# Performance work log

Measured on AMD Instinct MI355X. Metric: run time of the kernel, lower is better.

The kernel has to match this reference:

```python
import jax, jax.numpy as jnp
import numpy as np

B, S, D, H, DH = 2, 2048, 1024, 16, 64
LN_EPS = 1e-5

def _layernorm(x, g, b):
    mu = jnp.mean(x, axis=-1, keepdims=True)
    var = jnp.mean(jnp.square(x - mu), axis=-1, keepdims=True)
    return (x - mu) * jax.lax.rsqrt(var + LN_EPS) * g + b

def setup_inputs() -> dict:
    key = jax.random.key(0)
    ks = jax.random.split(key, 12)
    s = 0.02
    return {
        'x': jax.random.normal(ks[0], (B, S, D), jnp.float32),
        'attention_mask': jnp.zeros((B, S), jnp.bool_),
        'Wq': jax.random.normal(ks[1], (H, D, DH), jnp.float32) * s,
        'bq': jnp.zeros((H, DH), jnp.float32),
        'Wk': jax.random.normal(ks[2], (H, D, DH), jnp.float32) * s,
        'bk': jnp.zeros((H, DH), jnp.float32),
        'Wv': jax.random.normal(ks[3], (H, D, DH), jnp.float32) * s,
        'bv': jnp.zeros((H, DH), jnp.float32),
        'ln_g': jnp.ones((D,), jnp.float32),
        'ln_b': jnp.zeros((D,), jnp.float32),
        'W1': jax.random.normal(ks[4], (D, 4 * D), jnp.float32) * s,
        'b1': jnp.zeros((4 * D,), jnp.float32),
        'W2': jax.random.normal(ks[5], (4 * D, D), jnp.float32) * s,
        'b2': jnp.zeros((D,), jnp.float32),
    }

def reference(x, attention_mask, Wq, bq, Wk, bk, Wv, bv, ln_g, ln_b, W1, b1, W2, b2):
    # NOTE: source has a typo bug ('attentoin_score'), so the attention_mask is
    # computed-then-discarded; softmax is applied to the UNMASKED scaled scores.
    dh = Wq.shape[-1]
    q = jnp.einsum('bsd,hde->bhse', x, Wq) + bq[:, None, :]  # [B,H,S,dh]
    k = jnp.einsum('bsd,hde->bhse', x, Wk) + bk[:, None, :]
    v = jnp.einsum('bsd,hde->bhse', x, Wv) + bv[:, None, :]
    scores = jnp.einsum('bhse,bhte->bhst', q, k) / jnp.sqrt(jnp.float32(dh))
    attn = jax.nn.softmax(scores, axis=-1)
    o = jnp.einsum('bhst,bhte->bhse', attn, v)  # [B,H,S,dh]
    b_, h_, s_, e_ = o.shape
    # concat heads along last dim == transpose then reshape
    mha = jnp.transpose(o, (0, 2, 1, 3)).reshape(b_, s_, h_ * e_)
    h1 = _layernorm(x + mha, ln_g, ln_b)
    ffn = jax.nn.relu(h1 @ W1 + b1) @ W2 + b2
    return _layernorm(h1 + ffn, ln_g, ln_b)
```

## Files before the change

kernel.cpp:

```cpp
#include <hip/hip_runtime.h>

#define DEVI __device__ __forceinline__

typedef __attribute__((ext_vector_type(8))) __bf16 bf16x8;
typedef __attribute__((ext_vector_type(4))) float f32x4;
typedef __attribute__((ext_vector_type(4))) unsigned short u16x4;
typedef __attribute__((ext_vector_type(8))) unsigned short u16x8;

static DEVI unsigned short f2bf(float f) {
  unsigned int i = __float_as_uint(f);
  i += 0x7fffu + ((i >> 16) & 1u);
  return (unsigned short)(i >> 16);
}

static DEVI unsigned short f2bfh(float f) {
  union { __bf16 h; unsigned short u; } c;
  c.h = (__bf16)f;
  return c.u;
}

static DEVI float bf2f(unsigned short u) {
  return __uint_as_float((unsigned int)u << 16);
}

static DEVI f32x4 mfma16x16x32(bf16x8 a, bf16x8 b, f32x4 c) {
  return __builtin_amdgcn_mfma_f32_16x16x32_bf16(a, b, c, 0, 0, 0);
}

static DEVI void async_ld16(const void* g, void* lds) {
  __builtin_amdgcn_global_load_lds(
      (const __attribute__((address_space(1))) void*)g,
      (__attribute__((address_space(3))) void*)lds, 16, 0, 0);
}

template <int BN, int OUT_MODE, bool RELU>
static DEVI void gemm_bt_core(const unsigned short* __restrict__ A, int lda,
                              const unsigned short* __restrict__ Bt, int ldb,
                              int K, int m0, int n0,
                              const float* __restrict__ bias,
                              void* __restrict__ Cp, int ldc,
                              const float* __restrict__ bq,
                              const float* __restrict__ bk,
                              const float* __restrict__ bv,
                              unsigned short* __restrict__ qo,
                              unsigned short* __restrict__ ko,
                              unsigned short* __restrict__ vo) {
  constexpr int MT = (BN == 128) ? 4 : 2;
  constexpr int NT = 4;
  __shared__ __align__(16) unsigned short As[128 * 32];
  __shared__ __align__(16) unsigned short Bs[BN * 32];

  const int tid = threadIdx.x;
  const int w = tid >> 6, l = tid & 63;
  const int lr = l & 15, lq = l >> 4;
  const int wm0 = (BN == 128) ? ((w >> 1) * 64) : (w * 32);
  const int wn0 = (BN == 128) ? ((w & 1) * 64) : 0;
  const int lrow = l >> 2;
  const int lcol = (l & 3) * 8;

  f32x4 acc[MT][NT];
#pragma unroll
  for (int i = 0; i < MT; ++i)
#pragma unroll
    for (int j = 0; j < NT; ++j) acc[i][j] = (f32x4){0.f, 0.f, 0.f, 0.f};

  for (int kb = 0; kb < K; kb += 32) {
#pragma unroll
    for (int p = 0; p < 2; ++p) {
      const int r0 = p * 64 + w * 16;
      async_ld16(A + (size_t)(m0 + r0 + lrow) * lda + kb + lcol, As + r0 * 32);
    }
#pragma unroll
    for (int p = 0; p < BN / 64; ++p) {
      const int r0 = p * 64 + w * 16;
      async_ld16(Bt + (size_t)(n0 + r0 + lrow) * ldb + kb + lcol, Bs + r0 * 32);
    }
    __syncthreads();

    bf16x8 af[MT], bfr[NT];
#pragma unroll
    for (int mt = 0; mt < MT; ++mt)
      af[mt] = *(const bf16x8*)(As + (wm0 + mt * 16 + lr) * 32 + lq * 8);
#pragma unroll
    for (int nt = 0; nt < NT; ++nt)
      bfr[nt] = *(const bf16x8*)(Bs + (wn0 + nt * 16 + lr) * 32 + lq * 8);
#pragma unroll
    for (int mt = 0; mt < MT; ++mt)
#pragma unroll
      for (int nt = 0; nt < NT; ++nt)
        acc[mt][nt] = mfma16x16x32(af[mt], bfr[nt], acc[mt][nt]);
    __syncthreads();
  }

#pragma unroll
  for (int mt = 0; mt < MT; ++mt) {
    const int grow = m0 + wm0 + mt * 16 + lq * 4;
#pragma unroll
    for (int nt = 0; nt < NT; ++nt) {
      const int gcol = n0 + wn0 + nt * 16 + lr;
      if (OUT_MODE == 2) {
        const int which = gcol >> 10;
        const int h = (gcol >> 6) & 15;
        const int e = gcol & 63;
        const float* bp = (which == 0) ? bq : (which == 1) ? bk : bv;
        const float bvv = bp[gcol & 1023];
#pragma unroll
        for (int r = 0; r < 4; ++r) {
          const int row = grow + r;
          const int b_ = row >> 11, s_ = row & 2047;
          const size_t base = (size_t)((b_ << 4) + h) * 131072;
          const float val = acc[mt][nt][r] + bvv;
          if (which == 0) {
            qo[base + (size_t)s_ * 64 + e] = f2bf(val);
          } else if (which == 1) {
            const int o = e >> 3;
            const int pos = (((o ^ (s_ & 7)) << 3) | (e & 7));
            ko[base + (size_t)s_ * 64 + pos] = f2bf(val * 0.18033688011112f);
          } else {
            const int t = s_ >> 6, k64 = s_ & 63;
            const int kap = (k64 & 15) * 4 + (k64 >> 4);
            const int pos = (((kap >> 3) ^ (e & 7)) << 3) | (kap & 7);
            vo[base + (size_t)e * 2048 + t * 64 + pos] = f2bf(val);
          }
        }
      } else if (OUT_MODE == 3) {
#pragma unroll
        for (int r = 0; r < 4; ++r)
          ((unsigned short*)Cp)[(size_t)(grow + r) * ldc + gcol] =
              f2bf(acc[mt][nt][r]);
      } else {
        const float bvv = bias[gcol];
#pragma unroll
        for (int r = 0; r < 4; ++r) {
          float val = acc[mt][nt][r] + bvv;
          if (RELU) val = fmaxf(val, 0.f);
          if (OUT_MODE == 1)
            ((unsigned short*)Cp)[(size_t)(grow + r) * ldc + gcol] = f2bf(val);
          else
            ((float*)Cp)[(size_t)(grow + r) * ldc + gcol] = val;
        }
      }
    }
  }
}

__global__ __launch_bounds__(256) void k_gemm_qkv(
    const unsigned short* __restrict__ xb, const unsigned short* __restrict__ Wt,
    const float* __restrict__ bq, const float* __restrict__ bk,
    const float* __restrict__ bv, unsigned short* __restrict__ qo,
    unsigned short* __restrict__ ko, unsigned short* __restrict__ vo) {
  gemm_bt_core<128, 2, false>(xb, 1024, Wt, 1024, 1024, blockIdx.x * 128,
                              blockIdx.y * 128, nullptr, nullptr, 0, bq, bk, bv,
                              qo, ko, vo);
}

__global__ __launch_bounds__(256) void k_ffn1(
    const unsigned short* __restrict__ h1b, const unsigned short* __restrict__ W1t,
    const float* __restrict__ b1, unsigned short* __restrict__ f1) {
  gemm_bt_core<128, 1, true>(h1b, 1024, W1t, 1024, 1024, blockIdx.x * 128,
                             blockIdx.y * 128, b1, f1, 4096, nullptr, nullptr,
                             nullptr, nullptr, nullptr, nullptr);
}

__global__ __launch_bounds__(256) void k_ffn2(
    const unsigned short* __restrict__ f1, const unsigned short* __restrict__ W2t,
    unsigned short* __restrict__ pbase) {
  const int z = blockIdx.z;
  unsigned short* p = pbase + (size_t)z * 4194304;
  gemm_bt_core<128, 3, false>(f1 + z * 1024, 4096, W2t + z * 1024, 4096, 1024,
                              blockIdx.x * 128, blockIdx.y * 128, nullptr, p,
                              1024, nullptr, nullptr, nullptr, nullptr, nullptr,
                              nullptr);
}

static DEVI void tr64(const float* __restrict__ s, int sld,
                      unsigned short* __restrict__ d, int dld) {
  __shared__ float t[64][65];
  const int tr = threadIdx.x >> 4;
  const int tc4 = (threadIdx.x & 15) * 4;
#pragma unroll
  for (int i = 0; i < 4; ++i) {
    f32x4 v = *(const f32x4*)(s + (size_t)(i * 16 + tr) * sld + tc4);
#pragma unroll
    for (int j = 0; j < 4; ++j) t[i * 16 + tr][tc4 + j] = v[j];
  }
  __syncthreads();
#pragma unroll
  for (int i = 0; i < 4; ++i) {
    const int c = i * 16 + tr;
    u16x4 pk;
#pragma unroll
    for (int j = 0; j < 4; ++j) pk[j] = f2bf(t[tc4 + j][c]);
    *(u16x4*)(d + (size_t)c * dld + tc4) = pk;
  }
}

__global__ __launch_bounds__(256) void k_prep(
    const float* __restrict__ x, const float* __restrict__ Wq,
    const float* __restrict__ Wk, const float* __restrict__ Wv,
    const float* __restrict__ W1, const float* __restrict__ W2,
    unsigned short* __restrict__ xb, unsigned short* __restrict__ wqkvt,
    unsigned short* __restrict__ w1t, unsigned short* __restrict__ w2t) {
  const int bid = blockIdx.x;
  if (bid < 1024) {
    const size_t i0 = ((size_t)bid * 256 + threadIdx.x) * 16;
#pragma unroll
    for (int c = 0; c < 4; ++c) {
      f32x4 v = *(const f32x4*)(x + i0 + c * 4);
      u16x4 pk;
#pragma unroll
      for (int j = 0; j < 4; ++j) pk[j] = f2bf(v[j]);
      *(u16x4*)(xb + i0 + c * 4) = pk;
    }
  } else if (bid < 1792) {
    const int t = bid - 1024;
    const int bx = t & 15, by = t >> 4;
    const int which = by >> 4, h = by & 15;
    const float* W = (which == 0) ? Wq : (which == 1) ? Wk : Wv;
    const float* s = W + (size_t)h * 65536;
    unsigned short* d = wqkvt + (size_t)(which * 1024 + h * 64) * 1024;
    const int r0 = bx * 64;
    tr64(s + (size_t)r0 * 64, 64, d + r0, 1024);
  } else if (bid < 2816) {
    const int t = bid - 1792;
    const int bx = t & 15, by = t >> 4;
    const int r0 = bx * 64, c0 = by * 64;
    tr64(W1 + (size_t)r0 * 4096 + c0, 4096, w1t + (size_t)c0 * 1024 + r0, 1024);
  } else {
    const int t = bid - 2816;
    const int bx = t & 63, by = t >> 6;
    const int r0 = bx * 64, c0 = by * 64;
    tr64(W2 + (size_t)r0 * 1024 + c0, 1024, w2t + (size_t)c0 * 4096 + r0, 4096);
  }
}

__global__ __launch_bounds__(512) void k_attn(
    const unsigned short* __restrict__ q, const unsigned short* __restrict__ ks,
    const unsigned short* __restrict__ vp, unsigned short* __restrict__ mha) {
  const int bid = blockIdx.x;
  const int bh = (bid & 7) * 4 + ((bid >> 3) >> 4);
  const int qt = (bid >> 3) & 15;
  const int b = bh >> 4, h = bh & 15;
  const int tid = threadIdx.x;
  const int w = tid >> 6, l = tid & 63;
  const int lr = l & 15, lq = l >> 4, l7 = lr & 7;

  __shared__ __align__(16) unsigned short Ks[2][64 * 64];
  __shared__ __align__(16) unsigned short Vt[2][64 * 64];
  __shared__ __align__(16) unsigned short Ps[8][16][72];

  const size_t bho = (size_t)bh * 131072;
  const int q0 = qt * 128 + w * 16;

  bf16x8 qf0, qf1;
  {
    const unsigned short* qp = q + bho + (size_t)(q0 + lr) * 64 + lq * 8;
    qf0 = *(const bf16x8*)qp;
    qf1 = *(const bf16x8*)(qp + 32);
  }

  f32x4 l_acc[4];
  f32x4 o[4];
#pragma unroll
  for (int i = 0; i < 4; ++i) {
    l_acc[i] = (f32x4){0.f, 0.f, 0.f, 0.f};
    o[i] = (f32x4){0.f, 0.f, 0.f, 0.f};
  }

  const unsigned short* kg = ks + bho;
  const unsigned short* vg = vp + bho;
  const int srow = l >> 3, scol = (l & 7) * 8;
  const int r0 = w * 8;

  async_ld16(kg + (size_t)(r0 + srow) * 64 + scol, &Ks[0][r0 * 64]);
  async_ld16(vg + (size_t)(r0 + srow) * 2048 + scol, &Vt[0][r0 * 64]);
  __syncthreads();

  for (int kt = 0; kt < 32; ++kt) {
    const int cur = kt & 1, nxt = cur ^ 1;
    if (kt + 1 < 32) {
      const int k1 = (kt + 1) * 64;
      async_ld16(kg + (size_t)(k1 + r0 + srow) * 64 + scol, &Ks[nxt][r0 * 64]);
      async_ld16(vg + (size_t)(r0 + srow) * 2048 + k1 + scol, &Vt[nxt][r0 * 64]);
    }

    bf16x8 kf[4][2];
#pragma unroll
    for (int ct = 0; ct < 4; ++ct)
#pragma unroll
      for (int hh = 0; hh < 2; ++hh)
        kf[ct][hh] = *(const bf16x8*)&Ks[cur][(ct * 16 + lr) * 64 +
                                             (((hh << 2) | lq) ^ l7) * 8];
    f32x4 s[4];
#pragma unroll
    for (int ct = 0; ct < 4; ++ct) {
      f32x4 t = {0.f, 0.f, 0.f, 0.f};
      t = mfma16x16x32(qf0, kf[ct][0], t);
      t = mfma16x16x32(qf1, kf[ct][1], t);
      s[ct] = t;
    }

#pragma unroll
    for (int r = 0; r < 4; ++r) {
      f32x4 pe;
#pragma unroll
      for (int ct = 0; ct < 4; ++ct)
        pe[ct] = __builtin_amdgcn_exp2f(s[ct][r]);
      l_acc[r] += pe;
      u16x4 pk;
#pragma unroll
      for (int ct = 0; ct < 4; ++ct) pk[ct] = f2bfh(pe[ct]);
      *(u16x4*)&Ps[w][lq * 4 + r][lr * 4] = pk;
    }
    __asm__ volatile("" ::: "memory");

    bf16x8 vf[4][2];
#pragma unroll
    for (int dt = 0; dt < 4; ++dt)
#pragma unroll
      for (int hh = 0; hh < 2; ++hh)
        vf[dt][hh] = *(const bf16x8*)&Vt[cur][(dt * 16 + lr) * 64 +
                                             (((hh << 2) | lq) ^ l7) * 8];
    bf16x8 pf0 = *(const bf16x8*)&Ps[w][lr][lq * 8];
    bf16x8 pf1 = *(const bf16x8*)&Ps[w][lr][32 + lq * 8];
#pragma unroll
    for (int dt = 0; dt < 4; ++dt) {
      o[dt] = mfma16x16x32(pf0, vf[dt][0], o[dt]);
      o[dt] = mfma16x16x32(pf1, vf[dt][1], o[dt]);
    }
    __syncthreads();
  }

#pragma unroll
  for (int r = 0; r < 4; ++r) {
    f32x4 la = l_acc[r];
    float sd = la[0] + la[1] + la[2] + la[3];
    sd += __shfl_xor(sd, 1);
    sd += __shfl_xor(sd, 2);
    sd += __shfl_xor(sd, 4);
    sd += __shfl_xor(sd, 8);
    const float inv = 1.f / sd;
    unsigned short* op =
        mha + ((size_t)b * 2048 + q0 + lq * 4 + r) * 1024 + h * 64 + lr;
    op[0] = f2bfh(o[0][r] * inv);
    op[16] = f2bfh(o[1][r] * inv);
    op[32] = f2bfh(o[2][r] * inv);
    op[48] = f2bfh(o[3][r] * inv);
  }
}

__global__ __launch_bounds__(256) void k_add_ln(const float* __restrict__ a,
                                                const unsigned short* __restrict__ b,
                                                const float* __restrict__ g,
                                                const float* __restrict__ be,
                                                unsigned short* __restrict__ outb) {
  const int row = blockIdx.x;
  const int tid = threadIdx.x;
  const size_t base = (size_t)row * 1024 + tid * 4;
  f32x4 va = *(const f32x4*)(a + base);
  u16x4 ub = *(const u16x4*)(b + base);
  f32x4 xx;
  float s = 0.f, q = 0.f;
#pragma unroll
  for (int i = 0; i < 4; ++i) {
    xx[i] = va[i] + bf2f(ub[i]);
    s += xx[i];
    q += xx[i] * xx[i];
  }
#pragma unroll
  for (int off = 1; off < 64; off <<= 1) {
    s += __shfl_xor(s, off);
    q += __shfl_xor(q, off);
  }
  __shared__ float ss[4], qs[4];
  const int w = tid >> 6;
  if ((tid & 63) == 0) { ss[w] = s; qs[w] = q; }
  __syncthreads();
  s = ss[0] + ss[1] + ss[2] + ss[3];
  q = qs[0] + qs[1] + qs[2] + qs[3];
  const float mean = s * (1.f / 1024.f);
  const float var = q * (1.f / 1024.f) - mean * mean;
  const float rstd = rsqrtf(var + 1e-5f);
  f32x4 vg = *(const f32x4*)(g + tid * 4);
  f32x4 vbe = *(const f32x4*)(be + tid * 4);
  u16x4 pk;
#pragma unroll
  for (int i = 0; i < 4; ++i)
    pk[i] = f2bf((xx[i] - mean) * rstd * vg[i] + vbe[i]);
  *(u16x4*)(outb + base) = pk;
}

__global__ __launch_bounds__(256) void k_add_ln4(
    const unsigned short* __restrict__ h1b, const unsigned short* __restrict__ pb,
    const float* __restrict__ cb, const float* __restrict__ g,
    const float* __restrict__ be, float* __restrict__ out) {
  const int row = blockIdx.x;
  const int tid = threadIdx.x;
  const size_t base = (size_t)row * 1024 + tid * 4;
  u16x4 uh = *(const u16x4*)(h1b + base);
  u16x4 up[4];
#pragma unroll
  for (int z = 0; z < 4; ++z)
    up[z] = *(const u16x4*)(pb + base + (size_t)z * 4194304);
  f32x4 vcb = *(const f32x4*)(cb + tid * 4);
  f32x4 xx;
  float s = 0.f, q = 0.f;
#pragma unroll
  for (int i = 0; i < 4; ++i) {
    float v = bf2f(uh[i]) + vcb[i];
#pragma unroll
    for (int z = 0; z < 4; ++z) v += bf2f(up[z][i]);
    xx[i] = v;
    s += v;
    q += v * v;
  }
#pragma unroll
  for (int off = 1; off < 64; off <<= 1) {
    s += __shfl_xor(s, off);
    q += __shfl_xor(q, off);
  }
  __shared__ float ss[4], qs[4];
  const int w = tid >> 6;
  if ((tid & 63) == 0) { ss[w] = s; qs[w] = q; }
  __syncthreads();
  s = ss[0] + ss[1] + ss[2] + ss[3];
  q = qs[0] + qs[1] + qs[2] + qs[3];
  const float mean = s * (1.f / 1024.f);
  const float var = q * (1.f / 1024.f) - mean * mean;
  const float rstd = rsqrtf(var + 1e-5f);
  f32x4 vg = *(const f32x4*)(g + tid * 4);
  f32x4 vbe = *(const f32x4*)(be + tid * 4);
  f32x4 ov;
#pragma unroll
  for (int i = 0; i < 4; ++i) ov[i] = (xx[i] - mean) * rstd * vg[i] + vbe[i];
  *(f32x4*)(out + base) = ov;
}

extern "C" void kernel_launch(void* const* d_in, const int* in_sizes, int n_in,
                              void* d_out, int out_size, void* d_ws,
                              size_t ws_size, hipStream_t stream) {
  const float* x = (const float*)d_in[0];
  const float* Wq = (const float*)d_in[2];
  const float* bq = (const float*)d_in[3];
  const float* Wk = (const float*)d_in[4];
  const float* bk = (const float*)d_in[5];
  const float* Wv = (const float*)d_in[6];
  const float* bv = (const float*)d_in[7];
  const float* lg = (const float*)d_in[8];
  const float* lb = (const float*)d_in[9];
  const float* W1 = (const float*)d_in[10];
  const float* b1 = (const float*)d_in[11];
  const float* W2 = (const float*)d_in[12];
  const float* b2 = (const float*)d_in[13];

  char* ws = (char*)d_ws;
  const size_t MB = 1024 * 1024;
  unsigned short* qb = (unsigned short*)(ws + 0);
  unsigned short* kb = (unsigned short*)(ws + 8 * MB);
  unsigned short* vp = (unsigned short*)(ws + 16 * MB);
  unsigned short* f1 = (unsigned short*)(ws + 0);
  unsigned short* xb = (unsigned short*)(ws + 32 * MB);
  unsigned short* pb = (unsigned short*)(ws + 32 * MB);
  unsigned short* mha = (unsigned short*)(ws + 40 * MB);
  unsigned short* h1b = (unsigned short*)(ws + 64 * MB);
  unsigned short* wqkvt = (unsigned short*)(ws + 72 * MB);
  unsigned short* w1t = (unsigned short*)(ws + 78 * MB);
  unsigned short* w2t = (unsigned short*)(ws + 86 * MB);

  k_prep<<<dim3(3840), 256, 0, stream>>>(x, Wq, Wk, Wv, W1, W2, xb, wqkvt, w1t,
                                         w2t);
  k_gemm_qkv<<<dim3(32, 24), 256, 0, stream>>>(xb, wqkvt, bq, bk, bv, qb, kb, vp);
  k_attn<<<dim3(512), 512, 0, stream>>>(qb, kb, vp, mha);
  k_add_ln<<<dim3(4096), 256, 0, stream>>>(x, mha, lg, lb, h1b);
  k_ffn1<<<dim3(32, 32), 256, 0, stream>>>(h1b, w1t, b1, f1);
  k_ffn2<<<dim3(32, 8, 4), 256, 0, stream>>>(f1, w2t, pb);
  k_add_ln4<<<dim3(4096), 256, 0, stream>>>(h1b, pb, b2, lg, lb, (float*)d_out);
}
```

Before: 325.3 us.

## Replace GEMM core with 256x256 double-buffered pipelined tile and XCD-aware block mapping

Replaces the 128x128 single-buffered GEMM core with a 256x256 tile over 8 waves and a 64-wide K step. LDS is double-buffered and XOR-swizzled, async loads are interleaved with quadrant MFMA phases, and explicit vmcnt waits, barriers and setprio are used. Blocks are remapped so tiles sharing A/B rows land on the same XCD, aiming at higher arithmetic intensity, overlapped loads and better L2 reuse. The grid shrinks to 192/256/256 blocks, so wave quantization and occupancy with 128 KB LDS per block are risks.

```diff
diff --git a/kernel.cpp b/kernel.cpp
--- a/kernel.cpp
+++ b/kernel.cpp
@@ -33,11 +33,16 @@
       (__attribute__((address_space(3))) void*)lds, 16, 0, 0);
 }
 
-template <int BN, int OUT_MODE, bool RELU>
-static DEVI void gemm_bt_core(const unsigned short* __restrict__ A, int lda,
+static DEVI void wg_barrier() {
+  __asm__ volatile("" ::: "memory");
+  __builtin_amdgcn_s_barrier();
+  __asm__ volatile("" ::: "memory");
+}
+
+template <int OUT_MODE, bool RELU>
+static DEVI void gemm256_core(const unsigned short* __restrict__ A, int lda,
                               const unsigned short* __restrict__ Bt, int ldb,
-                              int K, int m0, int n0,
-                              const float* __restrict__ bias,
+                              int m0, int n0, const float* __restrict__ bias,
                               void* __restrict__ Cp, int ldc,
                               const float* __restrict__ bq,
                               const float* __restrict__ bk,
@@ -45,132 +50,213 @@
                               unsigned short* __restrict__ qo,
                               unsigned short* __restrict__ ko,
                               unsigned short* __restrict__ vo) {
-  constexpr int MT = (BN == 128) ? 4 : 2;
-  constexpr int NT = 4;
-  __shared__ __align__(16) unsigned short As[128 * 32];
-  __shared__ __align__(16) unsigned short Bs[BN * 32];
+  constexpr int NKT = 16;
+  __shared__ __align__(16) unsigned short As[2][16384];
+  __shared__ __align__(16) unsigned short Bs[2][16384];
 
   const int tid = threadIdx.x;
   const int w = tid >> 6, l = tid & 63;
   const int lr = l & 15, lq = l >> 4;
-  const int wm0 = (BN == 128) ? ((w >> 1) * 64) : (w * 32);
-  const int wn0 = (BN == 128) ? ((w & 1) * 64) : 0;
-  const int lrow = l >> 2;
-  const int lcol = (l & 3) * 8;
-
-  f32x4 acc[MT][NT];
-#pragma unroll
-  for (int i = 0; i < MT; ++i)
-#pragma unroll
-    for (int j = 0; j < NT; ++j) acc[i][j] = (f32x4){0.f, 0.f, 0.f, 0.f};
-
-  for (int kb = 0; kb < K; kb += 32) {
-#pragma unroll
-    for (int p = 0; p < 2; ++p) {
-      const int r0 = p * 64 + w * 16;
-      async_ld16(A + (size_t)(m0 + r0 + lrow) * lda + kb + lcol, As + r0 * 32);
-    }
-#pragma unroll
-    for (int p = 0; p < BN / 64; ++p) {
-      const int r0 = p * 64 + w * 16;
-      async_ld16(Bt + (size_t)(n0 + r0 + lrow) * ldb + kb + lcol, Bs + r0 * 32);
-    }
-    __syncthreads();
-
-    bf16x8 af[MT], bfr[NT];
-#pragma unroll
-    for (int mt = 0; mt < MT; ++mt)
-      af[mt] = *(const bf16x8*)(As + (wm0 + mt * 16 + lr) * 32 + lq * 8);
-#pragma unroll
-    for (int nt = 0; nt < NT; ++nt)
-      bfr[nt] = *(const bf16x8*)(Bs + (wn0 + nt * 16 + lr) * 32 + lq * 8);
-#pragma unroll
-    for (int mt = 0; mt < MT; ++mt)
-#pragma unroll
-      for (int nt = 0; nt < NT; ++nt)
-        acc[mt][nt] = mfma16x16x32(af[mt], bfr[nt], acc[mt][nt]);
-    __syncthreads();
-  }
-
-#pragma unroll
-  for (int mt = 0; mt < MT; ++mt) {
-    const int grow = m0 + wm0 + mt * 16 + lq * 4;
-#pragma unroll
-    for (int nt = 0; nt < NT; ++nt) {
-      const int gcol = n0 + wn0 + nt * 16 + lr;
-      if (OUT_MODE == 2) {
-        const int which = gcol >> 10;
-        const int h = (gcol >> 6) & 15;
-        const int e = gcol & 63;
-        const float* bp = (which == 0) ? bq : (which == 1) ? bk : bv;
-        const float bvv = bp[gcol & 1023];
-#pragma unroll
-        for (int r = 0; r < 4; ++r) {
-          const int row = grow + r;
-          const int b_ = row >> 11, s_ = row & 2047;
-          const size_t base = (size_t)((b_ << 4) + h) * 131072;
-          const float val = acc[mt][nt][r] + bvv;
-          if (which == 0) {
-            qo[base + (size_t)s_ * 64 + e] = f2bf(val);
-          } else if (which == 1) {
-            const int o = e >> 3;
-            const int pos = (((o ^ (s_ & 7)) << 3) | (e & 7));
-            ko[base + (size_t)s_ * 64 + pos] = f2bf(val * 0.18033688011112f);
+  const int wm = w >> 2, wn = w & 3;
+
+  const int srow = tid >> 3;
+  const int scol = ((tid & 7) ^ (srow & 7)) << 3;
+  const unsigned short* sA = A + (size_t)(m0 + srow) * lda + scol;
+  const unsigned short* sB = Bt + (size_t)(n0 + srow) * ldb + scol;
+  unsigned short* dA = &As[0][0] + w * 512;
+  unsigned short* dB = &Bs[0][0] + w * 512;
+
+  auto stA = [&](int c, int h, int kb) {
+    const unsigned short* s = sA + (size_t)h * 128 * lda + kb;
+    unsigned short* d = dA + c * 16384 + h * 8192;
+    async_ld16(s, d);
+    async_ld16(s + (size_t)64 * lda, d + 4096);
+  };
+  auto stB = [&](int c, int h, int kb) {
+    const unsigned short* s = sB + (size_t)h * 128 * ldb + kb;
+    unsigned short* d = dB + c * 16384 + h * 8192;
+    async_ld16(s, d);
+    async_ld16(s + (size_t)64 * ldb, d + 4096);
+  };
+
+  stA(0, 0, 0); stB(0, 0, 0); stB(0, 1, 0); stA(0, 1, 0);
+  stA(1, 0, 64); stB(1, 0, 64); stB(1, 1, 64);
+
+  f32x4 acc[8][4];
+#pragma unroll
+  for (int i = 0; i < 8; ++i)
+#pragma unroll
+    for (int j = 0; j < 4; ++j) acc[i][j] = (f32x4){0.f, 0.f, 0.f, 0.f};
+
+  const int frow = wm * 16 + lr;
+  const int brow = wn * 16 + lr;
+  const int g0 = (lq ^ (lr & 7)) << 3;
+  const int g1 = ((4 + lq) ^ (lr & 7)) << 3;
+
+  bf16x8 af[4][2], bf[2][2][2];
+
+  auto mfma_quad = [&](int qm, int qn) {
+    __builtin_amdgcn_s_setprio(1);
+#pragma unroll
+    for (int m = 0; m < 4; ++m)
+#pragma unroll
+      for (int n = 0; n < 2; ++n) {
+        f32x4 t = acc[qm * 4 + m][qn * 2 + n];
+        t = mfma16x16x32(af[m][0], bf[qn][n][0], t);
+        t = mfma16x16x32(af[m][1], bf[qn][n][1], t);
+        acc[qm * 4 + m][qn * 2 + n] = t;
+      }
+    __builtin_amdgcn_s_setprio(0);
+  };
+
+  asm volatile("s_waitcnt vmcnt(6)" ::: "memory");
+  wg_barrier();
+
+  for (int kt = 0; kt < NKT; ++kt) {
+    const int c = kt & 1;
+    const unsigned short* Ac = &As[c][0];
+    const unsigned short* Bc = &Bs[c][0];
+    const int kb1 = (kt + 1) * 64, kb2 = (kt + 2) * 64;
+
+#pragma unroll
+    for (int m = 0; m < 4; ++m) {
+      const unsigned short* p = Ac + (frow + m * 32) * 64;
+      af[m][0] = *(const bf16x8*)(p + g0);
+      af[m][1] = *(const bf16x8*)(p + g1);
+    }
+#pragma unroll
+    for (int n = 0; n < 2; ++n) {
+      const unsigned short* p = Bc + (brow + n * 64) * 64;
+      bf[0][n][0] = *(const bf16x8*)(p + g0);
+      bf[0][n][1] = *(const bf16x8*)(p + g1);
+    }
+    if (kt + 1 < NKT) stA(c ^ 1, 1, kb1);
+    wg_barrier();
+    mfma_quad(0, 0);
+    wg_barrier();
+
+#pragma unroll
+    for (int n = 0; n < 2; ++n) {
+      const unsigned short* p = Bc + (128 + brow + n * 64) * 64;
+      bf[1][n][0] = *(const bf16x8*)(p + g0);
+      bf[1][n][1] = *(const bf16x8*)(p + g1);
+    }
+    if (kt + 2 < NKT) stA(c, 0, kb2);
+    wg_barrier();
+    mfma_quad(0, 1);
+    wg_barrier();
+
+#pragma unroll
+    for (int m = 0; m < 4; ++m) {
+      const unsigned short* p = Ac + (128 + frow + m * 32) * 64;
+      af[m][0] = *(const bf16x8*)(p + g0);
+      af[m][1] = *(const bf16x8*)(p + g1);
+    }
+    if (kt + 2 < NKT) stB(c, 0, kb2);
+    wg_barrier();
+    mfma_quad(1, 0);
+    wg_barrier();
+
+    if (kt + 2 < NKT) stB(c, 1, kb2);
+    wg_barrier();
+    mfma_quad(1, 1);
+    if (kt < NKT - 2)
+      asm volatile("s_waitcnt vmcnt(6)" ::: "memory");
+    else
+      asm volatile("s_waitcnt vmcnt(0)" ::: "memory");
+    wg_barrier();
+  }
+
+#pragma unroll
+  for (int qm = 0; qm < 2; ++qm)
+#pragma unroll
+    for (int m = 0; m < 4; ++m) {
+      const int grow = m0 + qm * 128 + wm * 16 + m * 32 + lq * 4;
+#pragma unroll
+      for (int qn = 0; qn < 2; ++qn)
+#pragma unroll
+        for (int n = 0; n < 2; ++n) {
+          const int gcol = n0 + qn * 128 + wn * 16 + n * 64 + lr;
+          const f32x4 av = acc[qm * 4 + m][qn * 2 + n];
+          if (OUT_MODE == 2) {
+            const int which = gcol >> 10;
+            const int h = (gcol >> 6) & 15;
+            const int e = gcol & 63;
+            const float* bp = (which == 0) ? bq : (which == 1) ? bk : bv;
+            const float bvv = bp[gcol & 1023];
+#pragma unroll
+            for (int r = 0; r < 4; ++r) {
+              const int row = grow + r;
+              const int b_ = row >> 11, s_ = row & 2047;
+              const size_t base = (size_t)((b_ << 4) + h) * 131072;
+              const float val = av[r] + bvv;
+              if (which == 0) {
+                qo[base + (size_t)s_ * 64 + e] = f2bf(val);
+              } else if (which == 1) {
+                const int o = e >> 3;
+                const int pos = (((o ^ (s_ & 7)) << 3) | (e & 7));
+                ko[base + (size_t)s_ * 64 + pos] = f2bf(val * 0.18033688011112f);
+              } else {
+                const int t = s_ >> 6, k64 = s_ & 63;
+                const int kap = (k64 & 15) * 4 + (k64 >> 4);
+                const int pos = (((kap >> 3) ^ (e & 7)) << 3) | (kap & 7);
+                vo[base + (size_t)e * 2048 + t * 64 + pos] = f2bf(val);
+              }
+            }
+          } else if (OUT_MODE == 3) {
+#pragma unroll
+            for (int r = 0; r < 4; ++r)
+              ((unsigned short*)Cp)[(size_t)(grow + r) * ldc + gcol] =
+                  f2bf(av[r]);
           } else {
-            const int t = s_ >> 6, k64 = s_ & 63;
-            const int kap = (k64 & 15) * 4 + (k64 >> 4);
-            const int pos = (((kap >> 3) ^ (e & 7)) << 3) | (kap & 7);
-            vo[base + (size_t)e * 2048 + t * 64 + pos] = f2bf(val);
+            const float bvv = bias[gcol];
+#pragma unroll
+            for (int r = 0; r < 4; ++r) {
+              float val = av[r] + bvv;
+              if (RELU) val = fmaxf(val, 0.f);
+              ((unsigned short*)Cp)[(size_t)(grow + r) * ldc + gcol] = f2bf(val);
+            }
           }
         }
-      } else if (OUT_MODE == 3) {
-#pragma unroll
-        for (int r = 0; r < 4; ++r)
-          ((unsigned short*)Cp)[(size_t)(grow + r) * ldc + gcol] =
-              f2bf(acc[mt][nt][r]);
-      } else {
-        const float bvv = bias[gcol];
-#pragma unroll
-        for (int r = 0; r < 4; ++r) {
-          float val = acc[mt][nt][r] + bvv;
-          if (RELU) val = fmaxf(val, 0.f);
-          if (OUT_MODE == 1)
-            ((unsigned short*)Cp)[(size_t)(grow + r) * ldc + gcol] = f2bf(val);
-          else
-            ((float*)Cp)[(size_t)(grow + r) * ldc + gcol] = val;
-        }
-      }
-    }
-  }
-}
-
-__global__ __launch_bounds__(256) void k_gemm_qkv(
+    }
+}
+
+__global__ __launch_bounds__(512, 2) void k_gemm_qkv(
     const unsigned short* __restrict__ xb, const unsigned short* __restrict__ Wt,
     const float* __restrict__ bq, const float* __restrict__ bk,
     const float* __restrict__ bv, unsigned short* __restrict__ qo,
     unsigned short* __restrict__ ko, unsigned short* __restrict__ vo) {
-  gemm_bt_core<128, 2, false>(xb, 1024, Wt, 1024, 1024, blockIdx.x * 128,
-                              blockIdx.y * 128, nullptr, nullptr, 0, bq, bk, bv,
-                              qo, ko, vo);
-}
-
-__global__ __launch_bounds__(256) void k_ffn1(
+  const int bid = blockIdx.x;
+  const int xcd = bid & 7, idx = bid >> 3;
+  const int mt = (xcd >> 1) * 4 + idx / 6;
+  const int nt = (xcd & 1) * 6 + idx % 6;
+  gemm256_core<2, false>(xb, 1024, Wt, 1024, mt * 256, nt * 256, nullptr,
+                         nullptr, 0, bq, bk, bv, qo, ko, vo);
+}
+
+__global__ __launch_bounds__(512, 2) void k_ffn1(
     const unsigned short* __restrict__ h1b, const unsigned short* __restrict__ W1t,
     const float* __restrict__ b1, unsigned short* __restrict__ f1) {
-  gemm_bt_core<128, 1, true>(h1b, 1024, W1t, 1024, 1024, blockIdx.x * 128,
-                             blockIdx.y * 128, b1, f1, 4096, nullptr, nullptr,
-                             nullptr, nullptr, nullptr, nullptr);
-}
-
-__global__ __launch_bounds__(256) void k_ffn2(
+  const int bid = blockIdx.x;
+  const int xcd = bid & 7, idx = bid >> 3;
+  const int mt = (xcd >> 1) * 4 + (idx >> 3);
+  const int nt = (xcd & 1) * 8 + (idx & 7);
+  gemm256_core<1, true>(h1b, 1024, W1t, 1024, mt * 256, nt * 256, b1, f1, 4096,
+                        nullptr, nullptr, nullptr, nullptr, nullptr, nullptr);
+}
+
+__global__ __launch_bounds__(512, 2) void k_ffn2(
     const unsigned short* __restrict__ f1, const unsigned short* __restrict__ W2t,
     unsigned short* __restrict__ pbase) {
   const int z = blockIdx.z;
   unsigned short* p = pbase + (size_t)z * 4194304;
-  gemm_bt_core<128, 3, false>(f1 + z * 1024, 4096, W2t + z * 1024, 4096, 1024,
-                              blockIdx.x * 128, blockIdx.y * 128, nullptr, p,
-                              1024, nullptr, nullptr, nullptr, nullptr, nullptr,
-                              nullptr);
+  const int bid = blockIdx.x;
+  const int xcd = bid & 7, idx = bid >> 3;
+  const int mt = xcd * 2 + (idx >> 2);
+  const int nt = idx & 3;
+  gemm256_core<3, false>(f1 + z * 1024, 4096, W2t + z * 1024, 4096, mt * 256,
+                         nt * 256, nullptr, p, 1024, nullptr, nullptr, nullptr,
+                         nullptr, nullptr, nullptr);
 }
 
 static DEVI void tr64(const float* __restrict__ s, int sld,
@@ -469,10 +555,10 @@
 
   k_prep<<<dim3(3840), 256, 0, stream>>>(x, Wq, Wk, Wv, W1, W2, xb, wqkvt, w1t,
                                          w2t);
-  k_gemm_qkv<<<dim3(32, 24), 256, 0, stream>>>(xb, wqkvt, bq, bk, bv, qb, kb, vp);
+  k_gemm_qkv<<<dim3(192), 512, 0, stream>>>(xb, wqkvt, bq, bk, bv, qb, kb, vp);
   k_attn<<<dim3(512), 512, 0, stream>>>(qb, kb, vp, mha);
   k_add_ln<<<dim3(4096), 256, 0, stream>>>(x, mha, lg, lb, h1b);
-  k_ffn1<<<dim3(32, 32), 256, 0, stream>>>(h1b, w1t, b1, f1);
-  k_ffn2<<<dim3(32, 8, 4), 256, 0, stream>>>(f1, w2t, pb);
+  k_ffn1<<<dim3(256), 512, 0, stream>>>(h1b, w1t, b1, f1);
+  k_ffn2<<<dim3(64, 1, 4), 512, 0, stream>>>(f1, w2t, pb);
   k_add_ln4<<<dim3(4096), 256, 0, stream>>>(h1b, pb, b2, lg, lb, (float*)d_out);
 }
```

Result: faster. 306.3 us (-5.9%).
